# Kernel optimization log

Measured on AMD Instinct MI355X. Metric: run time of the kernel, lower is better.

Reference implementation:

```python
import jax, jax.numpy as jnp
import numpy as np

ALPHA = 20.0


def setup_inputs() -> dict:
    key = jax.random.key(0)
    k1, k2 = jax.random.split(key)
    N, C = 8192, 8
    output = jax.random.normal(k1, (N, C), dtype=jnp.float32)
    target = jax.random.randint(k2, (N,), 0, C, dtype=jnp.int64)
    return {"output": output, "target": target}


def reference(output, target):
    # output: [N, C] logits, target: [N] int labels in [0, C-1]
    probs = jax.nn.softmax(output, axis=1)
    dtype = probs.dtype
    C = output.shape[1]
    total_auc = jnp.zeros((), dtype)
    valid_count = jnp.zeros((), dtype)
    for class_idx in range(C):  # fixed small class loop, matches original
        p = probs[:, class_idx]                      # [N]
        pos = (target == class_idx).astype(dtype)    # [N]
        neg = 1.0 - pos                              # [N]
        n_pos = pos.sum()
        n_neg = neg.sum()
        # pairwise sigmoid(alpha * (p_i - p_j)) masked to (pos_i, neg_j) pairs
        s = jax.nn.sigmoid(ALPHA * (p[:, None] - p[None, :]))  # [N, N]
        pair_sum = jnp.einsum('i,ij,j->', pos, s, neg)
        valid = jnp.logical_and(n_pos > 0, n_neg > 0)
        mean_auc_c = jnp.where(valid, pair_sum / jnp.maximum(n_pos * n_neg, 1.0), 0.0)
        total_auc = total_auc + mean_auc_c
        valid_count = valid_count + valid.astype(dtype)
    loss = jnp.where(valid_count > 0, 1.0 - total_auc / jnp.maximum(valid_count, 1.0), 0.0)
    return loss
```

## Files before the change

kernel.cpp:

```cpp
#include <hip/hip_runtime.h>

#define SCALE 28.853900817779268f
#define L2E   1.4426950408889634f
#define M 2048
#define T 1024
#define CPC 32
#define QB (M/CPC)

__device__ __forceinline__ float fexp2(float x){ return __builtin_amdgcn_exp2f(x); }
__device__ __forceinline__ float frcp (float x){ return __builtin_amdgcn_rcpf(x); }

#define WRED64(x) { _Pragma("unroll") for (int _o = 32; _o; _o >>= 1) x += __shfl_down(x, _o, 64); }
#define ALOAD(p) __hip_atomic_load((p), __ATOMIC_RELAXED, __HIP_MEMORY_SCOPE_AGENT)

__global__ __launch_bounds__(1024)
void k_fused(const float* __restrict__ logits, const int* __restrict__ tgt,
             float* __restrict__ out, unsigned* __restrict__ ticket,
             float* __restrict__ gpart, int* __restrict__ ccnt, int N){
  const int b = blockIdx.x, NB = (int)gridDim.x;
  const int c = b >> 5, ch = b & (CPC-1);
  const int tid = threadIdx.x, lane = tid & 63, w = tid >> 6;
  const float invM = 1.0f / (float)M;

  __shared__ int   HP[M];
  __shared__ float g[2*M];
  __shared__ int   wnp[16];
  __shared__ float rw[16];
  __shared__ float scs[8];
  __shared__ int   lastflag;

  ((int2*)HP)[tid] = make_int2(0, 0);
  #pragma unroll
  for (int r = 0; r < 4; ++r){
    int idx = tid + 1024*r;
    if (idx < 2*M-1){
      float d = (float)(idx - (M-1));
      g[idx] = frcp(1.0f + fexp2(SCALE * d * invM));
    }
  }
  __syncthreads();

  const float4* l4 = (const float4*)logits;
  #pragma unroll 2
  for (int i = tid; i < N; i += T){
    float4 A = l4[2*i], B4 = l4[2*i+1];
    float e0=fexp2(A.x *L2E), e1=fexp2(A.y *L2E), e2=fexp2(A.z *L2E), e3=fexp2(A.w *L2E);
    float e4=fexp2(B4.x*L2E), e5=fexp2(B4.y*L2E), e6=fexp2(B4.z*L2E), e7=fexp2(B4.w*L2E);
    float s = ((e0+e1)+(e2+e3))+((e4+e5)+(e6+e7));
    float ec = e0;
    ec=(c==1)?e1:ec; ec=(c==2)?e2:ec; ec=(c==3)?e3:ec;
    ec=(c==4)?e4:ec; ec=(c==5)?e5:ec; ec=(c==6)?e6:ec; ec=(c==7)?e7:ec;
    float p = ec * frcp(s);
    int bin = min((int)(p * (float)M), M-1);
    int inc = 1 + ((tgt[i] == c) ? (1 << 16) : 0);
    atomicAdd(&HP[bin], inc);
  }
  __syncthreads();

  float Hj0, Hj1; int np_part;
  {
    const int hp0 = HP[tid], hp1 = HP[tid + T];
    const int p0 = hp0 >> 16, p1 = hp1 >> 16;
    np_part = p0 + p1;
    Hj0 = (float)((hp0 & 0xFFFF) - p0);
    Hj1 = (float)((hp1 & 0xFFFF) - p1);
  }
  WRED64(np_part)
  if (lane == 0) wnp[w] = np_part;

  float tot = 0.f;
  const int i0 = ch + (M-1) - tid;
  #pragma unroll 4
  for (int q = 0; q < QB; ++q){
    int Pki = HP[ch + CPC*q] >> 16;
    if (Pki == 0) continue;
    float g0 = g[i0 + CPC*q];
    float g1 = g[i0 + CPC*q - 1024];
    tot += (float)Pki * fmaf(Hj0, g0, Hj1 * g1);
  }
  WRED64(tot)
  if (lane == 0) rw[w] = tot;
  __syncthreads();
  if (tid == 0){
    float bt = 0.f;
    #pragma unroll
    for (int i = 0; i < 16; ++i) bt += rw[i];
    atomicExch(&gpart[b], bt);
    if (ch == 0){
      int snp = 0;
      #pragma unroll
      for (int i = 0; i < 16; ++i) snp += wnp[i];
      atomicExch(&ccnt[c], snp);
    }
    __threadfence();
    unsigned old = atomicAdd(ticket, 1u);
    lastflag = ((old % (unsigned)NB) == (unsigned)(NB - 1));
  }
  __syncthreads();
  if (!lastflag) return;

  if (tid == 0) __threadfence();
  __syncthreads();
  if (tid < 256){
    int c2 = tid >> 5, l = tid & 31;
    float s = ALOAD(&gpart[c2*CPC + l]);
    #pragma unroll
    for (int o = 16; o; o >>= 1) s += __shfl_down(s, o, 32);
    if (l == 0) scs[c2] = s;
  }
  __syncthreads();
  if (tid < 8){
    int np = ALOAD(&ccnt[tid]);
    int nn = N - np;
    bool valid = (np > 0 && nn > 0);
    float t = valid ? scs[tid] / ((float)np * (float)nn) : 0.f;
    float f = valid ? 1.f : 0.f;
    #pragma unroll
    for (int o = 4; o; o >>= 1){
      t += __shfl_down(t, o, 8);
      f += __shfl_down(f, o, 8);
    }
    if (tid == 0) out[0] = (f > 0.f) ? (1.0f - t / f) : 0.0f;
  }
}

extern "C" void kernel_launch(void* const* d_in, const int* in_sizes, int n_in,
                              void* d_out, int out_size, void* d_ws, size_t ws_size,
                              hipStream_t stream) {
    const float* logits = (const float*)d_in[0];
    const int*   tgt    = (const int*)d_in[1];
    float* out = (float*)d_out;
    int N = in_sizes[1];

    unsigned* ticket = (unsigned*)d_ws;
    float* gpart = (float*)d_ws + 32;
    int*   ccnt  = (int*)((float*)d_ws + 288);

    k_fused<<<8*CPC, T, 0, stream>>>(logits, tgt, out, ticket, gpart, ccnt, N);
}
```

Baseline: 18.72 us.

## Pack sigmoid table as parity-specific float2 pairs and cache positive counts in LDS

Each block now builds a 2048-entry float2 sigmoid table whose pairing is chosen by the chunk's parity, so the inner loop fetches both needed weights with one 64-bit LDS read instead of two scalar reads. Positive-count bins are staged into a small LDS array, then broadcast with readlane, which removes the per-iteration HP load and the data-dependent skip branch. The loop is fully unrolled into four accumulators to shorten dependency chains. Histogram reads use int2. In exchange, zero-count bins are no longer skipped and an extra barrier is added.

Measured after the change: 17.11 us (median of 2 runs). 1.09x faster.

```diff
diff --git a/kernel.cpp b/kernel.cpp
--- a/kernel.cpp
+++ b/kernel.cpp
@@ -9,6 +9,9 @@
 
 __device__ __forceinline__ float fexp2(float x){ return __builtin_amdgcn_exp2f(x); }
 __device__ __forceinline__ float frcp (float x){ return __builtin_amdgcn_rcpf(x); }
+__device__ __forceinline__ float Gfun(int x, float invM){
+  return frcp(1.0f + fexp2(SCALE * (float)(x - (M-1)) * invM));
+}
 
 #define WRED64(x) { _Pragma("unroll") for (int _o = 32; _o; _o >>= 1) x += __shfl_down(x, _o, 64); }
 #define ALOAD(p) __hip_atomic_load((p), __ATOMIC_RELAXED, __HIP_MEMORY_SCOPE_AGENT)
@@ -21,23 +24,21 @@
   const int c = b >> 5, ch = b & (CPC-1);
   const int tid = threadIdx.x, lane = tid & 63, w = tid >> 6;
   const float invM = 1.0f / (float)M;
+  const int s = ch & 1;
 
-  __shared__ int   HP[M];
-  __shared__ float g[2*M];
-  __shared__ int   wnp[16];
-  __shared__ float rw[16];
-  __shared__ float scs[8];
-  __shared__ int   lastflag;
+  __shared__ int    HP[M];
+  __shared__ float2 G2[M];
+  __shared__ int    Pkc[64];
+  __shared__ int    wnp[16];
+  __shared__ float  rw[16];
+  __shared__ float  scs[8];
+  __shared__ int    lastflag;
 
   ((int2*)HP)[tid] = make_int2(0, 0);
-  #pragma unroll
-  for (int r = 0; r < 4; ++r){
-    int idx = tid + 1024*r;
-    if (idx < 2*M-1){
-      float d = (float)(idx - (M-1));
-      g[idx] = frcp(1.0f + fexp2(SCALE * d * invM));
-    }
-  }
+  G2[tid]        = make_float2(Gfun(2*tid + s,          invM),
+                               Gfun(2*tid + s + 1,      invM));
+  G2[tid + 1024] = make_float2(Gfun(2*(tid+1024) + s,   invM),
+                               Gfun(2*(tid+1024) + s+1, invM));
   __syncthreads();
 
   const float4* l4 = (const float4*)logits;
@@ -46,11 +47,11 @@
     float4 A = l4[2*i], B4 = l4[2*i+1];
     float e0=fexp2(A.x *L2E), e1=fexp2(A.y *L2E), e2=fexp2(A.z *L2E), e3=fexp2(A.w *L2E);
     float e4=fexp2(B4.x*L2E), e5=fexp2(B4.y*L2E), e6=fexp2(B4.z*L2E), e7=fexp2(B4.w*L2E);
-    float s = ((e0+e1)+(e2+e3))+((e4+e5)+(e6+e7));
+    float sm = ((e0+e1)+(e2+e3))+((e4+e5)+(e6+e7));
     float ec = e0;
     ec=(c==1)?e1:ec; ec=(c==2)?e2:ec; ec=(c==3)?e3:ec;
     ec=(c==4)?e4:ec; ec=(c==5)?e5:ec; ec=(c==6)?e6:ec; ec=(c==7)?e7:ec;
-    float p = ec * frcp(s);
+    float p = ec * frcp(sm);
     int bin = min((int)(p * (float)M), M-1);
     int inc = 1 + ((tgt[i] == c) ? (1 << 16) : 0);
     atomicAdd(&HP[bin], inc);
@@ -59,25 +60,35 @@
 
   float Hj0, Hj1; int np_part;
   {
-    const int hp0 = HP[tid], hp1 = HP[tid + T];
-    const int p0 = hp0 >> 16, p1 = hp1 >> 16;
+    int2 hp = ((const int2*)HP)[tid];
+    int p0 = hp.x >> 16, p1 = hp.y >> 16;
     np_part = p0 + p1;
-    Hj0 = (float)((hp0 & 0xFFFF) - p0);
-    Hj1 = (float)((hp1 & 0xFFFF) - p1);
+    Hj0 = (float)((hp.x & 0xFFFF) - p0);
+    Hj1 = (float)((hp.y & 0xFFFF) - p1);
   }
+  if (tid < 64) Pkc[tid] = HP[ch + CPC*tid];
   WRED64(np_part)
   if (lane == 0) wnp[w] = np_part;
+  __syncthreads();
 
-  float tot = 0.f;
-  const int i0 = ch + (M-1) - tid;
-  #pragma unroll 4
-  for (int q = 0; q < QB; ++q){
-    int Pki = HP[ch + CPC*q] >> 16;
-    if (Pki == 0) continue;
-    float g0 = g[i0 + CPC*q];
-    float g1 = g[i0 + CPC*q - 1024];
-    tot += (float)Pki * fmaf(Hj0, g0, Hj1 * g1);
+  const int jb = ((2046 + ch - s) >> 1) - tid;
+  const int pkv = Pkc[lane];
+  float t0 = 0.f, t1 = 0.f, t2 = 0.f, t3 = 0.f;
+  #pragma unroll
+  for (int q = 0; q < QB; q += 4){
+    #pragma unroll
+    for (int u = 0; u < 4; ++u){
+      int pq = __builtin_amdgcn_readlane(pkv, q + u);
+      float Pk = (float)(pq >> 16);
+      float2 gg = G2[jb + 16*(q + u)];
+      float term = fmaf(Hj0, gg.y, Hj1 * gg.x);
+      if (u == 0) t0 = fmaf(Pk, term, t0);
+      if (u == 1) t1 = fmaf(Pk, term, t1);
+      if (u == 2) t2 = fmaf(Pk, term, t2);
+      if (u == 3) t3 = fmaf(Pk, term, t3);
+    }
   }
+  float tot = (t0 + t1) + (t2 + t3);
   WRED64(tot)
   if (lane == 0) rw[w] = tot;
   __syncthreads();
@@ -103,10 +114,10 @@
   __syncthreads();
   if (tid < 256){
     int c2 = tid >> 5, l = tid & 31;
-    float s = ALOAD(&gpart[c2*CPC + l]);
+    float sp = ALOAD(&gpart[c2*CPC + l]);
     #pragma unroll
-    for (int o = 16; o; o >>= 1) s += __shfl_down(s, o, 32);
-    if (l == 0) scs[c2] = s;
+    for (int o = 16; o; o >>= 1) sp += __shfl_down(sp, o, 32);
+    if (l == 0) scs[c2] = sp;
   }
   __syncthreads();
   if (tid < 8){
```
